# Optimization experiments

Measured on AMD Instinct MI355X. Metric: run time of the kernel, lower is better.

The kernel has to match this reference:

```python
import jax, jax.numpy as jnp
import numpy as np


def _cdist(a, b):
    # a: [B,J,D], b: [B,P,D] -> Euclidean distances [B,J,P]
    # matmul-based expansion, matching torch.cdist(p=2) default path
    a2 = jnp.sum(a * a, axis=-1)          # [B,J]
    b2 = jnp.sum(b * b, axis=-1)          # [B,P]
    ab = jnp.einsum('bjd,bpd->bjp', a, b)  # [B,J,P]
    sq = a2[:, :, None] + b2[:, None, :] - 2.0 * ab
    return jnp.sqrt(jnp.maximum(sq, 0.0))


def setup_inputs() -> dict:
    key = jax.random.key(0)
    k1, k2, k3 = jax.random.split(key, 3)
    B, J, P, D = 64, 42, 16384, 3
    pred_joints = jax.random.normal(k1, (B, J, D), dtype=jnp.float32)
    object_points = jax.random.normal(k2, (B, P, D), dtype=jnp.float32)
    gt_distance = jax.random.uniform(k3, (B, J), dtype=jnp.float32)
    return {"pred_joints": pred_joints, "object_points": object_points,
            "gt_distance": gt_distance}


def reference(pred_joints, object_points, gt_distance):
    pred_dist = _cdist(pred_joints, object_points)   # [B,J,P]
    min_val = jnp.min(pred_dist, axis=2)             # [B,J]
    return jnp.mean((min_val - gt_distance) ** 2)    # scalar MSE
```

## Files before the change

kernel.cpp:

```cpp
#include <hip/hip_runtime.h>
#include <math.h>

#define B   64
#define NJ  42
#define NP  16384
#define CHUNKS 8
#define PC  (NP / CHUNKS)
#define TPB 256
#define PPT (PC / TPB)
#define RSTRIDE 260

__global__ __launch_bounds__(TPB) void sdl_min_kernel(
    const float* __restrict__ joints,
    const float* __restrict__ pts,
    unsigned int* __restrict__ wmin)
{
    __shared__ __align__(16) float4 sj[NJ];
    __shared__ __align__(16) float  red[NJ * RSTRIDE];

    const int tid = threadIdx.x;
    const int b   = blockIdx.x / CHUNKS;
    const int ch  = blockIdx.x % CHUNKS;

    if (tid < NJ) {
        const float* jp = joints + (b * NJ + tid) * 3;
        float x = jp[0], y = jp[1], z = jp[2];
        sj[tid] = make_float4(x, y, z, fmaf(x, x, fmaf(y, y, z * z)));
    }
    __syncthreads();

    float px[PPT], py[PPT], pz[PPT], p2[PPT];
    const float* pb = pts + (size_t)(b * NP + ch * PC) * 3;
#pragma unroll
    for (int k = 0; k < PPT; ++k) {
        int idx = (k * TPB + tid) * 3;
        float x = pb[idx], y = pb[idx + 1], z = pb[idx + 2];
        px[k] = x; py[k] = y; pz[k] = z;
        p2[k] = fmaf(x, x, fmaf(y, y, z * z));
    }

    float m[NJ];
#pragma unroll
    for (int j = 0; j < NJ; ++j) m[j] = 3.0e38f;

#pragma unroll
    for (int j = 0; j < NJ; ++j) {
        float4 Jv = sj[j];
#pragma unroll
        for (int k = 0; k < PPT; ++k) {
            float s = fmaf(px[k], Jv.x, fmaf(py[k], Jv.y, pz[k] * Jv.z));
            float v = fmaf(-2.0f, s, p2[k]);
            m[j] = fminf(m[j], v);
        }
    }

#pragma unroll
    for (int j = 0; j < NJ; ++j) red[j * RSTRIDE + tid] = m[j];
    __syncthreads();

    if (tid < NJ) {
        const float4* row = (const float4*)(red + tid * RSTRIDE);
        float4 a = row[0];
        for (int i = 1; i < TPB / 4; ++i) {
            float4 v = row[i];
            a.x = fminf(a.x, v.x); a.y = fminf(a.y, v.y);
            a.z = fminf(a.z, v.z); a.w = fminf(a.w, v.w);
        }
        float mn = fminf(fminf(a.x, a.y), fminf(a.z, a.w));
        float d2 = fmaxf(mn + sj[tid].w, 0.0f);
        atomicMin(wmin + b * NJ + tid, __float_as_uint(d2));
    }
}

__global__ __launch_bounds__(256) void sdl_final_kernel(
    const unsigned int* __restrict__ wmin,
    const float* __restrict__ gt,
    float* __restrict__ out)
{
    const int tid = threadIdx.x;
    float acc = 0.0f;
    for (int i = tid; i < B * NJ; i += 256) {
        float d    = sqrtf(__uint_as_float(wmin[i]));
        float diff = d - gt[i];
        acc = fmaf(diff, diff, acc);
    }
#pragma unroll
    for (int off = 32; off > 0; off >>= 1)
        acc += __shfl_xor(acc, off);
    __shared__ float wsum[4];
    if ((tid & 63) == 0) wsum[tid >> 6] = acc;
    __syncthreads();
    if (tid == 0)
        out[0] = (wsum[0] + wsum[1] + wsum[2] + wsum[3]) * (1.0f / (B * NJ));
}

extern "C" void kernel_launch(void* const* d_in, const int* in_sizes, int n_in,
                              void* d_out, int out_size, void* d_ws, size_t ws_size,
                              hipStream_t stream) {
    const float* pred = (const float*)d_in[0];
    const float* obj  = (const float*)d_in[1];
    const float* gt   = (const float*)d_in[2];
    unsigned int* wmin = (unsigned int*)d_ws;

    hipMemsetAsync(wmin, 0x7F, B * NJ * sizeof(unsigned int), stream);
    sdl_min_kernel<<<B * CHUNKS, TPB, 0, stream>>>(pred, obj, wmin);
    sdl_final_kernel<<<1, 256, 0, stream>>>(wmin, gt, (float*)d_out);
}
```

Baseline: 77.25 us.

## Use packed float2 FMA in min loop and replace atomic/memset with partial buffers

Pairs points into 2-wide float vectors with pre-negated coordinates and a halved squared norm, so each joint-point distance takes three packed FMAs and a min. This targets packed FP32 instructions. It also drops the workspace memset and atomicMin, writing per-chunk minima to a partial buffer that the final kernel reduces with 1024 threads. The barrier is moved after the point loads to overlap global loads with the joint setup.

```diff
diff --git a/kernel.cpp b/kernel.cpp
--- a/kernel.cpp
+++ b/kernel.cpp
@@ -8,36 +8,44 @@
 #define PC  (NP / CHUNKS)
 #define TPB 256
 #define PPT (PC / TPB)
+#define NPAIR (PPT / 2)
 #define RSTRIDE 260
+
+typedef float v2f __attribute__((ext_vector_type(2)));
 
 __global__ __launch_bounds__(TPB) void sdl_min_kernel(
     const float* __restrict__ joints,
     const float* __restrict__ pts,
-    unsigned int* __restrict__ wmin)
+    float* __restrict__ part)
 {
     __shared__ __align__(16) float4 sj[NJ];
     __shared__ __align__(16) float  red[NJ * RSTRIDE];
 
     const int tid = threadIdx.x;
-    const int b   = blockIdx.x / CHUNKS;
-    const int ch  = blockIdx.x % CHUNKS;
+    const int b   = blockIdx.x >> 3;
+    const int ch  = blockIdx.x & 7;
 
     if (tid < NJ) {
         const float* jp = joints + (b * NJ + tid) * 3;
         float x = jp[0], y = jp[1], z = jp[2];
         sj[tid] = make_float4(x, y, z, fmaf(x, x, fmaf(y, y, z * z)));
     }
-    __syncthreads();
 
-    float px[PPT], py[PPT], pz[PPT], p2[PPT];
+    v2f npx[NPAIR], npy[NPAIR], npz[NPAIR], q[NPAIR];
     const float* pb = pts + (size_t)(b * NP + ch * PC) * 3;
 #pragma unroll
-    for (int k = 0; k < PPT; ++k) {
-        int idx = (k * TPB + tid) * 3;
-        float x = pb[idx], y = pb[idx + 1], z = pb[idx + 2];
-        px[k] = x; py[k] = y; pz[k] = z;
-        p2[k] = fmaf(x, x, fmaf(y, y, z * z));
+    for (int k = 0; k < NPAIR; ++k) {
+        int i0 = ((2 * k)     * TPB + tid) * 3;
+        int i1 = ((2 * k + 1) * TPB + tid) * 3;
+        float x0 = pb[i0], y0 = pb[i0 + 1], z0 = pb[i0 + 2];
+        float x1 = pb[i1], y1 = pb[i1 + 1], z1 = pb[i1 + 2];
+        npx[k] = (v2f){-x0, -x1};
+        npy[k] = (v2f){-y0, -y1};
+        npz[k] = (v2f){-z0, -z1};
+        q[k]   = (v2f){0.5f * fmaf(x0, x0, fmaf(y0, y0, z0 * z0)),
+                       0.5f * fmaf(x1, x1, fmaf(y1, y1, z1 * z1))};
     }
+    __syncthreads();
 
     float m[NJ];
 #pragma unroll
@@ -46,12 +54,18 @@
 #pragma unroll
     for (int j = 0; j < NJ; ++j) {
         float4 Jv = sj[j];
+        v2f jx = (v2f){Jv.x, Jv.x};
+        v2f jy = (v2f){Jv.y, Jv.y};
+        v2f jz = (v2f){Jv.z, Jv.z};
+        float mj = m[j];
 #pragma unroll
-        for (int k = 0; k < PPT; ++k) {
-            float s = fmaf(px[k], Jv.x, fmaf(py[k], Jv.y, pz[k] * Jv.z));
-            float v = fmaf(-2.0f, s, p2[k]);
-            m[j] = fminf(m[j], v);
+        for (int k = 0; k < NPAIR; ++k) {
+            v2f t = npz[k] * jz + q[k];
+            t     = npy[k] * jy + t;
+            t     = npx[k] * jx + t;
+            mj = fminf(fminf(mj, t.x), t.y);
         }
+        m[j] = mj;
     }
 
 #pragma unroll
@@ -67,31 +81,37 @@
             a.z = fminf(a.z, v.z); a.w = fminf(a.w, v.w);
         }
         float mn = fminf(fminf(a.x, a.y), fminf(a.z, a.w));
-        float d2 = fmaxf(mn + sj[tid].w, 0.0f);
-        atomicMin(wmin + b * NJ + tid, __float_as_uint(d2));
+        float d2 = fmaxf(fmaf(2.0f, mn, sj[tid].w), 0.0f);
+        part[ch * (B * NJ) + b * NJ + tid] = d2;
     }
 }
 
-__global__ __launch_bounds__(256) void sdl_final_kernel(
-    const unsigned int* __restrict__ wmin,
+__global__ __launch_bounds__(1024) void sdl_final_kernel(
+    const float* __restrict__ part,
     const float* __restrict__ gt,
     float* __restrict__ out)
 {
     const int tid = threadIdx.x;
     float acc = 0.0f;
-    for (int i = tid; i < B * NJ; i += 256) {
-        float d    = sqrtf(__uint_as_float(wmin[i]));
-        float diff = d - gt[i];
+    for (int i = tid; i < B * NJ; i += 1024) {
+        float mn = part[i];
+#pragma unroll
+        for (int c = 1; c < CHUNKS; ++c) mn = fminf(mn, part[c * (B * NJ) + i]);
+        float diff = sqrtf(mn) - gt[i];
         acc = fmaf(diff, diff, acc);
     }
 #pragma unroll
     for (int off = 32; off > 0; off >>= 1)
         acc += __shfl_xor(acc, off);
-    __shared__ float wsum[4];
+    __shared__ float wsum[16];
     if ((tid & 63) == 0) wsum[tid >> 6] = acc;
     __syncthreads();
-    if (tid == 0)
-        out[0] = (wsum[0] + wsum[1] + wsum[2] + wsum[3]) * (1.0f / (B * NJ));
+    if (tid == 0) {
+        float s = 0.0f;
+#pragma unroll
+        for (int w = 0; w < 16; ++w) s += wsum[w];
+        out[0] = s * (1.0f / (B * NJ));
+    }
 }
 
 extern "C" void kernel_launch(void* const* d_in, const int* in_sizes, int n_in,
@@ -100,9 +120,8 @@
     const float* pred = (const float*)d_in[0];
     const float* obj  = (const float*)d_in[1];
     const float* gt   = (const float*)d_in[2];
-    unsigned int* wmin = (unsigned int*)d_ws;
+    float* part = (float*)d_ws;
 
-    hipMemsetAsync(wmin, 0x7F, B * NJ * sizeof(unsigned int), stream);
-    sdl_min_kernel<<<B * CHUNKS, TPB, 0, stream>>>(pred, obj, wmin);
-    sdl_final_kernel<<<1, 256, 0, stream>>>(wmin, gt, (float*)d_out);
+    sdl_min_kernel<<<B * CHUNKS, TPB, 0, stream>>>(pred, obj, part);
+    sdl_final_kernel<<<1, 1024, 0, stream>>>(part, gt, (float*)d_out);
 }
```

Measured after the change: 73.12 us. 1.06x faster.
